# Optimization experiments

Measured on AMD Instinct MI355X. Metric: run time of the kernel, lower is better.

## Reference

```python
import jax, jax.numpy as jnp
import numpy as np

K = 7          # kernel_size
PAD = K // 2   # padding


def _unfold(t):
    """im2col for kxk neighborhood: (B,C,H,W) -> (B,C,K*K,H,W), zero-padded."""
    B, C, H, W = t.shape
    p = jnp.pad(t, ((0, 0), (0, 0), (PAD, PAD), (PAD, PAD)))
    # row-major over kernel offsets matches F.unfold ordering
    wins = jnp.stack([p[:, :, i:i + H, j:j + W]
                      for i in range(K) for j in range(K)], axis=2)
    return wins


def setup_inputs() -> dict:
    key = jax.random.key(0)
    ks = jax.random.split(key, 7)
    B, C, H, W = 8, 128, 64, 64
    scale = 1.0 / np.sqrt(C)
    x = jax.random.normal(ks[0], (B, C, H, W), dtype=jnp.float32)
    Wq = jax.random.normal(ks[1], (C, C), dtype=jnp.float32) * scale
    Wk = jax.random.normal(ks[2], (C, C), dtype=jnp.float32) * scale
    Wv = jax.random.normal(ks[3], (C, C), dtype=jnp.float32) * scale
    bq = jax.random.normal(ks[4], (C,), dtype=jnp.float32) * 0.01
    bk = jax.random.normal(ks[5], (C,), dtype=jnp.float32) * 0.01
    bv = jax.random.normal(ks[6], (C,), dtype=jnp.float32) * 0.01
    return {"x": x, "Wq": Wq, "bq": bq, "Wk": Wk, "bk": bk, "Wv": Wv, "bv": bv}


def reference(x, Wq, bq, Wk, bk, Wv, bv):
    # 1x1 convs = channel GEMMs
    q = jnp.einsum('oc,bchw->bohw', Wq, x) + bq[:, None, None]
    k = jnp.einsum('oc,bchw->bohw', Wk, x) + bk[:, None, None]
    v = jnp.einsum('oc,bchw->bohw', Wv, x) + bv[:, None, None]
    k_unf = _unfold(k)   # (B,C,K*K,H,W)
    v_unf = _unfold(v)   # (B,C,K*K,H,W)
    # attention scores over the K*K neighborhood, summed over channels
    attn = jnp.einsum('bchw,bcphw->bphw', q, k_unf)
    attn = jax.nn.softmax(attn, axis=1)
    y = jnp.einsum('bphw,bcphw->bchw', attn, v_unf)
    return y
```

## Files before the change

### kernel.cpp

```cpp
#include <hip/hip_runtime.h>

#define CC   128
#define HH_  64
#define WW_  64
#define BB   8
#define HWSZ (HH_*WW_)
#define CHW  (CC*HWSZ)
#define BCHW (BB*CHW)
#define PAD  3
#define NP   49

__global__ __launch_bounds__(128) void qkv_proj(
    const float* __restrict__ x,
    const float* __restrict__ Wq, const float* __restrict__ bq,
    const float* __restrict__ Wk, const float* __restrict__ bk,
    const float* __restrict__ Wv, const float* __restrict__ bv,
    float* __restrict__ qkv)
{
    __shared__ float xs[32][132];
    __shared__ float ws[32][68];
    const int pt  = blockIdx.x;
    const int og  = blockIdx.y;
    const int b   = pt >> 5;
    const int hw0 = (pt & 31) << 7;
    const int tid = threadIdx.x;

    const int proj = og >> 1;
    const int row0 = (og & 1) << 6;
    const float* Wp = (proj == 0) ? Wq : (proj == 1 ? Wk : Wv);
    const float* Bp = (proj == 0) ? bq : (proj == 1 ? bk : bv);

    const int o8  = (tid >> 4) << 3;
    const int px4 = (tid & 15) << 2;

    float acc[8][8];
    #pragma unroll
    for (int j = 0; j < 8; ++j) {
        float bj = Bp[row0 + o8 + j];
        #pragma unroll
        for (int i = 0; i < 8; ++i) acc[j][i] = bj;
    }

    const float* xb = x + (size_t)b*CHW + hw0;

    for (int ck = 0; ck < 4; ++ck) {
        const int c0 = ck << 5;
        __syncthreads();
        #pragma unroll
        for (int i = 0; i < 8; ++i) {
            int f  = tid + (i << 7);
            int c  = f >> 5, q4 = (f & 31) << 2;
            *(float4*)&xs[c][q4] = *(const float4*)&xb[(size_t)(c0 + c)*HWSZ + q4];
        }
        #pragma unroll
        for (int i = 0; i < 4; ++i) {
            int f = tid + (i << 7);
            int o = f >> 3, c4 = (f & 7) << 2;
            float4 wv = *(const float4*)&Wp[(size_t)(row0 + o)*CC + c0 + c4];
            ws[c4+0][o] = wv.x; ws[c4+1][o] = wv.y;
            ws[c4+2][o] = wv.z; ws[c4+3][o] = wv.w;
        }
        __syncthreads();

        #pragma unroll 8
        for (int c = 0; c < 32; ++c) {
            float4 w0 = *(const float4*)&ws[c][o8];
            float4 w1 = *(const float4*)&ws[c][o8 + 4];
            float4 x0 = *(const float4*)&xs[c][px4];
            float4 x1 = *(const float4*)&xs[c][px4 + 64];
            float wr[8] = {w0.x,w0.y,w0.z,w0.w,w1.x,w1.y,w1.z,w1.w};
            float xr[8] = {x0.x,x0.y,x0.z,x0.w,x1.x,x1.y,x1.z,x1.w};
            #pragma unroll
            for (int j = 0; j < 8; ++j)
                #pragma unroll
                for (int i = 0; i < 8; ++i)
                    acc[j][i] = fmaf(wr[j], xr[i], acc[j][i]);
        }
    }

    float* op = qkv + (size_t)proj*BCHW + (size_t)b*CHW + hw0;
    #pragma unroll
    for (int j = 0; j < 8; ++j) {
        const int row = row0 + o8 + j;
        float4 s0 = make_float4(acc[j][0], acc[j][1], acc[j][2], acc[j][3]);
        float4 s1 = make_float4(acc[j][4], acc[j][5], acc[j][6], acc[j][7]);
        *(float4*)&op[(size_t)row*HWSZ + px4]      = s0;
        *(float4*)&op[(size_t)row*HWSZ + px4 + 64] = s1;
    }
}

__device__ __forceinline__ void load_chunk(const float* __restrict__ src,
                                           int h, int c0, float4* stg) {
    const int tid = threadIdx.x;
    #pragma unroll
    for (int i = 0; i < 7; ++i) {
        int f   = tid + (i << 8);
        int c   = f / 112;
        int rem = f - c*112;
        int r   = rem >> 4;
        int q4  = (rem & 15) << 2;
        int hh  = h + r - PAD;
        if ((unsigned)hh < (unsigned)HH_)
            stg[i] = *(const float4*)&src[(size_t)(c0 + c)*HWSZ + hh*WW_ + q4];
        else
            stg[i] = make_float4(0.f, 0.f, 0.f, 0.f);
    }
}

__device__ __forceinline__ void store_chunk(float (*ks)[7][72], const float4* stg) {
    const int tid = threadIdx.x;
    #pragma unroll
    for (int i = 0; i < 7; ++i) {
        int f   = tid + (i << 8);
        int c   = f / 112;
        int rem = f - c*112;
        int r   = rem >> 4;
        int q4  = (rem & 15) << 2;
        *(float4*)&ks[c][r][4 + q4] = stg[i];
    }
}

__global__ __launch_bounds__(256) void locatt(
    const float* __restrict__ qkv, float* __restrict__ out)
{
    __shared__ float ks[16][7][72];
    __shared__ float qs[16][64];
    __shared__ float lg[NP][64];
    __shared__ float dn[64];

    const int b   = blockIdx.x >> 6;
    const int h   = blockIdx.x & 63;
    const int tid = threadIdx.x;
    const int s   = tid >> 6;
    const int w   = tid & 63;

    const float* qp = qkv + (size_t)b*CHW;
    const float* kp = qkv + BCHW + (size_t)b*CHW;
    const float* vp = qkv + (size_t)2*BCHW + (size_t)b*CHW;

    if (tid < 224) {
        int cr  = tid % 112;
        int c   = cr / 7, r = cr % 7;
        int col = (tid < 112) ? 0 : 68;
        *(float4*)&ks[c][r][col] = make_float4(0.f, 0.f, 0.f, 0.f);
    }

    const int p0 = (NP * s) >> 2;
    const int p1 = (NP * (s + 1)) >> 2;
    const int np = p1 - p0;
    int offs[13];
    #pragma unroll
    for (int j = 0; j < 13; ++j) {
        int p = p0 + j; if (p > NP - 1) p = NP - 1;
        offs[j] = (p / 7) * 72 + (p % 7);
    }

    float accp[13];
    #pragma unroll
    for (int j = 0; j < 13; ++j) accp[j] = 0.f;

    float4 stg[7];
    float4 qstg;
    load_chunk(kp, h, 0, stg);
    {
        int c = tid >> 4, q4 = (tid & 15) << 2;
        qstg = *(const float4*)&qp[(size_t)c*HWSZ + h*WW_ + q4];
    }

    for (int ck = 0; ck < 8; ++ck) {
        store_chunk(ks, stg);
        {
            int c = tid >> 4, q4 = (tid & 15) << 2;
            *(float4*)&qs[c][q4] = qstg;
        }
        __syncthreads();
        if (ck < 7) {
            load_chunk(kp, h, (ck + 1) * 16, stg);
            int c = tid >> 4, q4 = (tid & 15) << 2;
            qstg = *(const float4*)&qp[(size_t)((ck + 1)*16 + c)*HWSZ + h*WW_ + q4];
        }
        float qreg[16];
        const float* qb = &qs[0][w];
        #pragma unroll
        for (int ci = 0; ci < 16; ++ci) qreg[ci] = qb[ci * 64];
        const float* kb = &ks[0][0][w + 1];
        #pragma unroll
        for (int j = 0; j < 13; ++j) {
            if (j < np) {
                const float* kr = kb + offs[j];
                #pragma unroll
                for (int ci = 0; ci < 16; ++ci)
                    accp[j] = fmaf(qreg[ci], kr[ci * 504], accp[j]);
            }
        }
        __syncthreads();
    }
    #pragma unroll
    for (int j = 0; j < 13; ++j)
        if (j < np) lg[p0 + j][w] = accp[j];
    __syncthreads();

    if (tid < 64) {
        float tv[NP];
        float m = -1e30f;
        #pragma unroll
        for (int p = 0; p < NP; ++p) { tv[p] = lg[p][tid]; m = fmaxf(m, tv[p]); }
        float d = 0.f;
        #pragma unroll
        for (int p = 0; p < NP; ++p) {
            float e = __expf(tv[p] - m);
            d += e;
            lg[p][tid] = e;
        }
        dn[tid] = 1.f / d;
    }
    __syncthreads();

    float a[NP];
    #pragma unroll
    for (int p = 0; p < NP; ++p) a[p] = lg[p][w];
    const float sc = dn[w];
    #pragma unroll
    for (int p = 0; p < NP; ++p) a[p] *= sc;

    load_chunk(vp, h, 0, stg);
    const int cbase = s << 2;
    for (int ck = 0; ck < 8; ++ck) {
        store_chunk(ks, stg);
        __syncthreads();
        if (ck < 7) load_chunk(vp, h, (ck + 1) * 16, stg);
        const float* kb = &ks[0][0][w + 1];
        #pragma unroll
        for (int ci = 0; ci < 4; ++ci) {
            const float* kr = kb + (cbase + ci) * 504;
            float acc = 0.f;
            #pragma unroll
            for (int p = 0; p < NP; ++p)
                acc = fmaf(a[p], kr[(p / 7) * 72 + (p % 7)], acc);
            out[(size_t)b*CHW + (size_t)(ck*16 + cbase + ci)*HWSZ + h*WW_ + w] = acc;
        }
        __syncthreads();
    }
}

extern "C" void kernel_launch(void* const* d_in, const int* in_sizes, int n_in,
                              void* d_out, int out_size, void* d_ws, size_t ws_size,
                              hipStream_t stream) {
    const float* x  = (const float*)d_in[0];
    const float* Wq = (const float*)d_in[1];
    const float* bq = (const float*)d_in[2];
    const float* Wk = (const float*)d_in[3];
    const float* bk = (const float*)d_in[4];
    const float* Wv = (const float*)d_in[5];
    const float* bv = (const float*)d_in[6];
    float* out = (float*)d_out;
    float* qkv = (float*)d_ws;

    qkv_proj<<<dim3(256, 6), 128, 0, stream>>>(x, Wq, bq, Wk, bk, Wv, bv, qkv);
    locatt  <<<BB*HH_, 256, 0, stream>>>(qkv, out);
}
```

Baseline: 162.3 us.

## Process two output rows per block in local attention to share K/V halo tiles

The attention kernel now handles two adjacent image rows per 512-thread block and stages an 8-row K/V window, so the 7-row halo is shared between the two rows. Each thread row-slice computes the logits for both output rows from each shared-memory K value. Q is read straight from global memory instead of being staged in shared memory. Block indices are remapped so that blocks with the same batch index are interleaved across rows. This cuts redundant K/V global loads by roughly half, at the cost of more registers (two 49-float attention arrays) and fewer blocks in the grid.

```diff
diff --git a/kernel.cpp b/kernel.cpp
--- a/kernel.cpp
+++ b/kernel.cpp
@@ -89,17 +89,17 @@
     }
 }
 
-__device__ __forceinline__ void load_chunk(const float* __restrict__ src,
-                                           int h, int c0, float4* stg) {
-    const int tid = threadIdx.x;
-    #pragma unroll
-    for (int i = 0; i < 7; ++i) {
-        int f   = tid + (i << 8);
-        int c   = f / 112;
-        int rem = f - c*112;
+__device__ __forceinline__ void load_chunk8(const float* __restrict__ src,
+                                            int h0, int c0, float4* stg) {
+    const int tid = threadIdx.x;
+    #pragma unroll
+    for (int i = 0; i < 4; ++i) {
+        int f   = tid + (i << 9);
+        int c   = f >> 7;
+        int rem = f & 127;
         int r   = rem >> 4;
         int q4  = (rem & 15) << 2;
-        int hh  = h + r - PAD;
+        int hh  = h0 - PAD + r;
         if ((unsigned)hh < (unsigned)HH_)
             stg[i] = *(const float4*)&src[(size_t)(c0 + c)*HWSZ + hh*WW_ + q4];
         else
@@ -107,137 +107,139 @@
     }
 }
 
-__device__ __forceinline__ void store_chunk(float (*ks)[7][72], const float4* stg) {
-    const int tid = threadIdx.x;
-    #pragma unroll
-    for (int i = 0; i < 7; ++i) {
-        int f   = tid + (i << 8);
-        int c   = f / 112;
-        int rem = f - c*112;
+__device__ __forceinline__ void store_chunk8(float (*ks)[8][72], const float4* stg) {
+    const int tid = threadIdx.x;
+    #pragma unroll
+    for (int i = 0; i < 4; ++i) {
+        int f   = tid + (i << 9);
+        int c   = f >> 7;
+        int rem = f & 127;
         int r   = rem >> 4;
         int q4  = (rem & 15) << 2;
         *(float4*)&ks[c][r][4 + q4] = stg[i];
     }
 }
 
-__global__ __launch_bounds__(256) void locatt(
+__global__ __launch_bounds__(512) void locatt(
     const float* __restrict__ qkv, float* __restrict__ out)
 {
-    __shared__ float ks[16][7][72];
-    __shared__ float qs[16][64];
-    __shared__ float lg[NP][64];
-    __shared__ float dn[64];
-
-    const int b   = blockIdx.x >> 6;
-    const int h   = blockIdx.x & 63;
+    __shared__ float ks[16][8][72];
+    __shared__ float lg[2][NP][64];
+    __shared__ float dn[2][64];
+
+    const int blk = blockIdx.x;
+    const int x   = blk & 7;
+    const int j   = blk >> 3;
+    const int b   = j >> 2;
+    const int h0  = (((x << 2) | (j & 3)) << 1);
     const int tid = threadIdx.x;
     const int s   = tid >> 6;
     const int w   = tid & 63;
 
     const float* qp = qkv + (size_t)b*CHW;
-    const float* kp = qkv + BCHW + (size_t)b*CHW;
+    const float* kp = qkv + (size_t)BCHW + (size_t)b*CHW;
     const float* vp = qkv + (size_t)2*BCHW + (size_t)b*CHW;
 
-    if (tid < 224) {
-        int cr  = tid % 112;
-        int c   = cr / 7, r = cr % 7;
-        int col = (tid < 112) ? 0 : 68;
+    if (tid < 256) {
+        int idx = tid & 127;
+        int c = idx >> 3, r = idx & 7;
+        int col = (tid < 128) ? 0 : 68;
         *(float4*)&ks[c][r][col] = make_float4(0.f, 0.f, 0.f, 0.f);
     }
 
-    const int p0 = (NP * s) >> 2;
-    const int p1 = (NP * (s + 1)) >> 2;
-    const int np = p1 - p0;
-    int offs[13];
-    #pragma unroll
-    for (int j = 0; j < 13; ++j) {
-        int p = p0 + j; if (p > NP - 1) p = NP - 1;
-        offs[j] = (p / 7) * 72 + (p % 7);
-    }
-
-    float accp[13];
-    #pragma unroll
-    for (int j = 0; j < 13; ++j) accp[j] = 0.f;
-
-    float4 stg[7];
-    float4 qstg;
-    load_chunk(kp, h, 0, stg);
-    {
-        int c = tid >> 4, q4 = (tid & 15) << 2;
-        qstg = *(const float4*)&qp[(size_t)c*HWSZ + h*WW_ + q4];
-    }
+    const bool do0 = (s < 7);
+    const bool do1 = (s >= 1);
+
+    float acc0[7], acc1[7];
+    #pragma unroll
+    for (int dx = 0; dx < 7; ++dx) { acc0[dx] = 0.f; acc1[dx] = 0.f; }
+
+    float4 stg[4];
+    load_chunk8(kp, h0, 0, stg);
 
     for (int ck = 0; ck < 8; ++ck) {
-        store_chunk(ks, stg);
-        {
-            int c = tid >> 4, q4 = (tid & 15) << 2;
-            *(float4*)&qs[c][q4] = qstg;
-        }
-        __syncthreads();
-        if (ck < 7) {
-            load_chunk(kp, h, (ck + 1) * 16, stg);
-            int c = tid >> 4, q4 = (tid & 15) << 2;
-            qstg = *(const float4*)&qp[(size_t)((ck + 1)*16 + c)*HWSZ + h*WW_ + q4];
-        }
-        float qreg[16];
-        const float* qb = &qs[0][w];
-        #pragma unroll
-        for (int ci = 0; ci < 16; ++ci) qreg[ci] = qb[ci * 64];
-        const float* kb = &ks[0][0][w + 1];
-        #pragma unroll
-        for (int j = 0; j < 13; ++j) {
-            if (j < np) {
-                const float* kr = kb + offs[j];
-                #pragma unroll
-                for (int ci = 0; ci < 16; ++ci)
-                    accp[j] = fmaf(qreg[ci], kr[ci * 504], accp[j]);
+        store_chunk8(ks, stg);
+        __syncthreads();
+        if (ck < 7) load_chunk8(kp, h0, (ck + 1) * 16, stg);
+
+        const int c0 = ck << 4;
+        float q0[16], q1[16];
+        #pragma unroll
+        for (int ci = 0; ci < 16; ++ci) {
+            const float* qc = qp + (size_t)(c0 + ci)*HWSZ + h0*WW_ + w;
+            q0[ci] = do0 ? qc[0]   : 0.f;
+            q1[ci] = do1 ? qc[WW_] : 0.f;
+        }
+
+        const float* kbase = &ks[0][s][w + 1];
+        #pragma unroll
+        for (int ci = 0; ci < 16; ++ci) {
+            const float* kc = kbase + ci * 576;
+            #pragma unroll
+            for (int dx = 0; dx < 7; ++dx) {
+                float kv = kc[dx];
+                acc0[dx] = fmaf(q0[ci], kv, acc0[dx]);
+                acc1[dx] = fmaf(q1[ci], kv, acc1[dx]);
             }
         }
         __syncthreads();
     }
-    #pragma unroll
-    for (int j = 0; j < 13; ++j)
-        if (j < np) lg[p0 + j][w] = accp[j];
+
+    #pragma unroll
+    for (int dx = 0; dx < 7; ++dx) {
+        if (do0) lg[0][s*7 + dx][w]       = acc0[dx];
+        if (do1) lg[1][(s-1)*7 + dx][w]   = acc1[dx];
+    }
+    load_chunk8(vp, h0, 0, stg);
     __syncthreads();
 
-    if (tid < 64) {
+    if (tid < 128) {
+        const int r = tid >> 6, px = tid & 63;
         float tv[NP];
         float m = -1e30f;
         #pragma unroll
-        for (int p = 0; p < NP; ++p) { tv[p] = lg[p][tid]; m = fmaxf(m, tv[p]); }
+        for (int p = 0; p < NP; ++p) { tv[p] = lg[r][p][px]; m = fmaxf(m, tv[p]); }
         float d = 0.f;
         #pragma unroll
         for (int p = 0; p < NP; ++p) {
             float e = __expf(tv[p] - m);
             d += e;
-            lg[p][tid] = e;
-        }
-        dn[tid] = 1.f / d;
+            lg[r][p][px] = e;
+        }
+        dn[r][px] = 1.f / d;
     }
     __syncthreads();
 
-    float a[NP];
-    #pragma unroll
-    for (int p = 0; p < NP; ++p) a[p] = lg[p][w];
-    const float sc = dn[w];
-    #pragma unroll
-    for (int p = 0; p < NP; ++p) a[p] *= sc;
-
-    load_chunk(vp, h, 0, stg);
-    const int cbase = s << 2;
+    float a0[NP], a1[NP];
+    const float sc0 = dn[0][w], sc1 = dn[1][w];
+    #pragma unroll
+    for (int p = 0; p < NP; ++p) a0[p] = lg[0][p][w] * sc0;
+    #pragma unroll
+    for (int p = 0; p < NP; ++p) a1[p] = lg[1][p][w] * sc1;
+
     for (int ck = 0; ck < 8; ++ck) {
-        store_chunk(ks, stg);
-        __syncthreads();
-        if (ck < 7) load_chunk(vp, h, (ck + 1) * 16, stg);
-        const float* kb = &ks[0][0][w + 1];
-        #pragma unroll
-        for (int ci = 0; ci < 4; ++ci) {
-            const float* kr = kb + (cbase + ci) * 504;
-            float acc = 0.f;
+        store_chunk8(ks, stg);
+        __syncthreads();
+        if (ck < 7) load_chunk8(vp, h0, (ck + 1) * 16, stg);
+
+        #pragma unroll
+        for (int half = 0; half < 2; ++half) {
+            const int cl = s + (half << 3);
+            float y0 = 0.f, y1 = 0.f;
             #pragma unroll
-            for (int p = 0; p < NP; ++p)
-                acc = fmaf(a[p], kr[(p / 7) * 72 + (p % 7)], acc);
-            out[(size_t)b*CHW + (size_t)(ck*16 + cbase + ci)*HWSZ + h*WW_ + w] = acc;
+            for (int r = 0; r < 8; ++r) {
+                const float* vr = &ks[cl][r][w + 1];
+                #pragma unroll
+                for (int dx = 0; dx < 7; ++dx) {
+                    float vv = vr[dx];
+                    if (r < 7)  y0 = fmaf(a0[r*7 + dx], vv, y0);
+                    if (r >= 1) y1 = fmaf(a1[(r-1)*7 + dx], vv, y1);
+                }
+            }
+            float* op = out + (size_t)b*CHW + (size_t)(ck*16 + cl)*HWSZ
+                            + (size_t)h0*WW_ + w;
+            op[0]   = y0;
+            op[WW_] = y1;
         }
         __syncthreads();
     }
@@ -257,5 +259,5 @@
     float* qkv = (float*)d_ws;
 
     qkv_proj<<<dim3(256, 6), 128, 0, stream>>>(x, Wq, bq, Wk, bk, Wv, bv, qkv);
-    locatt  <<<BB*HH_, 256, 0, stream>>>(qkv, out);
-}
+    locatt  <<<256, 512, 0, stream>>>(qkv, out);
+}
```

Measured after the change: 150.8 us. -7.1%, faster.
